# Optimization experiments

Measured on AMD Instinct MI355X. Metric: run time of the kernel, lower is better.

Reference implementation:

```python
import jax, jax.numpy as jnp
import numpy as np

B = 4          # per_gpu_batch_size
P = 16         # n_contexts
N = B * P      # fused passage dim = 64
L = 512        # seq_len
H = 768        # hidden_size
S = 16         # sentence spans per passage


def setup_inputs() -> dict:
    key = jax.random.key(0)
    k1, k2, k3 = jax.random.split(key, 3)
    hidden_states = jax.random.normal(k1, (N, L, H), jnp.float32)
    # nn.Linear weight [out, in]; original init std=1.0 saturates tanh, use 0.02 scale for sane numerics
    dense_w = jax.random.normal(k2, (H, H), jnp.float32) * 0.02
    dense_b = jnp.zeros((H,), jnp.float32)
    attention_mask = jnp.ones((N, L), jnp.int32)
    # strictly increasing boundaries -> S non-empty, ragged, contiguous spans per passage
    r = jnp.sort(jax.random.randint(k3, (N, S + 1), 0, L - S), axis=-1) + jnp.arange(S + 1, dtype=jnp.int32)
    spans = jnp.stack([r[:, :-1], r[:, 1:]], axis=-1).astype(jnp.int32)  # [N, S, 2]
    return dict(hidden_states=hidden_states, dense_w=dense_w, dense_b=dense_b,
                attention_mask=attention_mask, spans=spans)


def reference(hidden_states, dense_w, dense_b, attention_mask, spans):
    # sentence_spans branch: token_tensor = hidden_states (all tokens)
    # pooled_output = activation(dense(token_tensor)); cls_norm_type == 'none' -> no norm
    pooled = jnp.tanh(jnp.einsum('nlh,oh->nlo', hidden_states, dense_w) + dense_b)  # [N, L, H]
    pooled_output_passages = pooled[:, 0]  # [N, H]
    # ragged per-span mean pooling, vectorized as a masked segment reduce
    pos = jnp.arange(L, dtype=jnp.int32)                         # [L]
    start = spans[..., 0][..., None]                             # [N, S, 1]
    end = spans[..., 1][..., None]                               # [N, S, 1]
    m = ((pos >= start) & (pos < end)).astype(pooled.dtype)      # [N, S, L]
    sums = jnp.einsum('nsl,nlh->nsh', m, pooled)                 # [N, S, H]
    counts = (spans[..., 1] - spans[..., 0]).astype(pooled.dtype)[..., None]  # [N, S, 1]
    sentence_embeddings = (sums / counts).reshape(N * S, H)      # [N*S, H]
    # all S spans valid per passage -> mask of zeros (0 = valid in original code)
    sentence_mask = jnp.zeros((N, S), jnp.float32)
    return pooled_output_passages, sentence_embeddings, sentence_mask
```

## Files before the change

kernel.cpp:

```cpp
#include <hip/hip_runtime.h>
#include <hip/hip_bf16.h>

#define NPASS 64
#define LSEQ  512
#define HDIM  768
#define NSPAN 16
#define OFF_SENT (NPASS*HDIM)
#define OFF_MASK (OFF_SENT + NPASS*NSPAN*HDIM)

#define BN   96
#define NTN  6
#define BK   32
#define NK   (HDIM/BK)
#define NTILES (HDIM/BN)
#define NBLK (NPASS*NTILES)
#define THREADS 1024
#define NMT  2

typedef __bf16 bf16x8 __attribute__((ext_vector_type(8)));
typedef __bf16 bf16x4 __attribute__((ext_vector_type(4)));
typedef float  f32x4  __attribute__((ext_vector_type(4)));

__device__ inline float fast_tanh(float x) {
  const float ax = fabsf(x);
  const float t  = __expf(-2.0f * ax);
  const float r  = (1.0f - t) * __builtin_amdgcn_rcpf(1.0f + t);
  return copysignf(r, x);
}

__device__ inline bf16x8 cvt8(f32x4 lo, f32x4 hi) {
  union { bf16x4 h[2]; bf16x8 v; } u;
  u.h[0] = __builtin_convertvector(lo, bf16x4);
  u.h[1] = __builtin_convertvector(hi, bf16x4);
  return u.v;
}

__global__ __launch_bounds__(THREADS, 4) void fused_kernel(
    const float* __restrict__ A,
    const float* __restrict__ W,
    const float* __restrict__ bias,
    const int*   __restrict__ spans,
    float* __restrict__ out)
{
  __shared__ __align__(16) unsigned short Wl[BN * HDIM];
  __shared__ float sent_lds[NSPAN][BN];
  __shared__ float inv_s[NSPAN];
  __shared__ float bias_s[BN];
  __shared__ short sid_l[LSEQ];

  const int tid = threadIdx.x;
  const int b   = blockIdx.x;
  const int xcd = b & 7;
  const int t   = b >> 3;
  const int p   = ((t >> 3) << 3) | xcd;
  const int ntb = t & 7;
  const int tile_n = ntb * BN;


  {
    const float* Wp = W + (size_t)tile_n * HDIM;
    #pragma unroll
    for (int j = 0; j < (BN * (HDIM / 8)) / THREADS; ++j) {
      const int g  = j * THREADS + tid;
      const int wr = g / (HDIM / 8);
      const int kg = g % (HDIM / 8);
      const float* src = Wp + (size_t)wr * HDIM + kg * 8;
      const f32x4 lo = *(const f32x4*)src;
      const f32x4 hi = *(const f32x4*)(src + 4);
      const int kgs = kg ^ (wr & 7);
      *(bf16x8*)(Wl + (size_t)wr * HDIM + kgs * 8) = cvt8(lo, hi);
    }
  }

  if (tid < LSEQ) {
    int st[NSPAN], en[NSPAN];
    #pragma unroll
    for (int i = 0; i < NSPAN; ++i) {
      st[i] = spans[(p * NSPAN + i) * 2 + 0];
      en[i] = spans[(p * NSPAN + i) * 2 + 1];
    }
    short s = -1;
    #pragma unroll
    for (int i = 0; i < NSPAN; ++i)
      if (tid >= st[i] && tid < en[i]) s = (short)i;
    sid_l[tid] = s;
  }
  if (tid < NSPAN)
    inv_s[tid] = 1.0f / (float)(spans[(p * NSPAN + tid) * 2 + 1] -
                                spans[(p * NSPAN + tid) * 2 + 0]);
  if (tid >= 512 && tid < 512 + BN) bias_s[tid - 512] = bias[tile_n + tid - 512];
  for (int i = tid; i < NSPAN * BN; i += THREADS) (&sent_lds[0][0])[i] = 0.f;

  __syncthreads();

  const int wave = tid >> 6;
  const int lane = tid & 63;
  const int quad = lane >> 4;
  const int lr   = lane & 15;

  const float* Ab = A + ((size_t)p * LSEQ + wave * 32 + lr) * HDIM + quad * 8;

  f32x4 acc[NMT][NTN];
  #pragma unroll
  for (int mt = 0; mt < NMT; ++mt)
    #pragma unroll
    for (int nt = 0; nt < NTN; ++nt)
      acc[mt][nt] = (f32x4){0.f, 0.f, 0.f, 0.f};

  f32x4 alo[NMT], ahi[NMT];
  #pragma unroll
  for (int mt = 0; mt < NMT; ++mt) {
    const float* s0 = Ab + (size_t)mt * 16 * HDIM;
    alo[mt] = *(const f32x4*)s0;
    ahi[mt] = *(const f32x4*)(s0 + 4);
  }

  #pragma unroll
  for (int k = 0; k < NK; ++k) {
    bf16x8 wf[NTN];
    #pragma unroll
    for (int nt = 0; nt < NTN; ++nt) {
      const int wr = nt * 16 + lr;
      const int kg = (4 * k + quad) ^ (lr & 7);
      wf[nt] = *(const bf16x8*)(Wl + (size_t)wr * HDIM + kg * 8);
    }
    bf16x8 abf[NMT];
    #pragma unroll
    for (int mt = 0; mt < NMT; ++mt) abf[mt] = cvt8(alo[mt], ahi[mt]);
    if (k + 1 < NK) {
      #pragma unroll
      for (int mt = 0; mt < NMT; ++mt) {
        const float* s1 = Ab + (size_t)mt * 16 * HDIM + (k + 1) * BK;
        alo[mt] = *(const f32x4*)s1;
        ahi[mt] = *(const f32x4*)(s1 + 4);
      }
    }
    __builtin_amdgcn_s_setprio(1);
    #pragma unroll
    for (int mt = 0; mt < NMT; ++mt)
      #pragma unroll
      for (int nt = 0; nt < NTN; ++nt)
        acc[mt][nt] = __builtin_amdgcn_mfma_f32_16x16x32_bf16(
            abf[mt], wf[nt], acc[mt][nt], 0, 0, 0);
    __builtin_amdgcn_s_setprio(0);
  }

  #pragma unroll
  for (int nt = 0; nt < NTN; ++nt) {
    const int col = nt * 16 + lr;
    const float bv = bias_s[col];
    #pragma unroll
    for (int mt = 0; mt < NMT; ++mt) {
      const int rowbase = wave * 32 + mt * 16 + quad * 4;
      int prev = -1; float run = 0.f;
      #pragma unroll
      for (int r = 0; r < 4; ++r) {
        const int row = rowbase + r;
        const float v = fast_tanh(acc[mt][nt][r] + bv);
        if (row == 0) out[(size_t)p * HDIM + tile_n + col] = v;
        const int s = sid_l[row];
        if (s != prev) {
          if (prev >= 0) atomicAdd(&sent_lds[prev][col], run);
          prev = s; run = 0.f;
        }
        run += v;
      }
      if (prev >= 0) atomicAdd(&sent_lds[prev][col], run);
    }
  }
  __syncthreads();

  for (int i = tid; i < NSPAN * BN; i += THREADS) {
    const int s = i / BN, c = i % BN;
    out[OFF_SENT + ((size_t)p * NSPAN + s) * HDIM + tile_n + c] =
        sent_lds[s][c] * inv_s[s];
  }
  if (ntb == 0 && tid < NSPAN) out[OFF_MASK + p * NSPAN + tid] = 0.f;
}

extern "C" void kernel_launch(void* const* d_in, const int* in_sizes, int n_in,
                              void* d_out, int out_size, void* d_ws, size_t ws_size,
                              hipStream_t stream) {
  const float* hs  = (const float*)d_in[0];
  const float* w   = (const float*)d_in[1];
  const float* bsc = (const float*)d_in[2];
  const int* spans = (const int*)d_in[4];

  fused_kernel<<<dim3(NBLK), dim3(THREADS), 0, stream>>>(
      hs, w, bsc, spans, (float*)d_out);
}
```

Baseline: 228.8 us.

## Replace LDS atomic span accumulation with fp16 tile staging and serial span sums

```diff
diff --git a/kernel.cpp b/kernel.cpp
--- a/kernel.cpp
+++ b/kernel.cpp
@@ -1,5 +1,6 @@
 #include <hip/hip_runtime.h>
 #include <hip/hip_bf16.h>
+#include <hip/hip_fp16.h>
 
 #define NPASS 64
 #define LSEQ  512
@@ -16,6 +17,7 @@
 #define NBLK (NPASS*NTILES)
 #define THREADS 1024
 #define NMT  2
+#define PSTR 516
 
 typedef __bf16 bf16x8 __attribute__((ext_vector_type(8)));
 typedef __bf16 bf16x4 __attribute__((ext_vector_type(4)));
@@ -43,10 +45,9 @@
     float* __restrict__ out)
 {
   __shared__ __align__(16) unsigned short Wl[BN * HDIM];
-  __shared__ float sent_lds[NSPAN][BN];
+  __shared__ int   sp_st[NSPAN], sp_en[NSPAN];
   __shared__ float inv_s[NSPAN];
   __shared__ float bias_s[BN];
-  __shared__ short sid_l[LSEQ];
 
   const int tid = threadIdx.x;
   const int b   = blockIdx.x;
@@ -72,24 +73,13 @@
     }
   }
 
-  if (tid < LSEQ) {
-    int st[NSPAN], en[NSPAN];
-    #pragma unroll
-    for (int i = 0; i < NSPAN; ++i) {
-      st[i] = spans[(p * NSPAN + i) * 2 + 0];
-      en[i] = spans[(p * NSPAN + i) * 2 + 1];
-    }
-    short s = -1;
-    #pragma unroll
-    for (int i = 0; i < NSPAN; ++i)
-      if (tid >= st[i] && tid < en[i]) s = (short)i;
-    sid_l[tid] = s;
+  if (tid < NSPAN) {
+    const int st = spans[(p * NSPAN + tid) * 2 + 0];
+    const int en = spans[(p * NSPAN + tid) * 2 + 1];
+    sp_st[tid] = st; sp_en[tid] = en;
+    inv_s[tid] = 1.0f / (float)(en - st);
   }
-  if (tid < NSPAN)
-    inv_s[tid] = 1.0f / (float)(spans[(p * NSPAN + tid) * 2 + 1] -
-                                spans[(p * NSPAN + tid) * 2 + 0]);
   if (tid >= 512 && tid < 512 + BN) bias_s[tid - 512] = bias[tile_n + tid - 512];
-  for (int i = tid; i < NSPAN * BN; i += THREADS) (&sent_lds[0][0])[i] = 0.f;
 
   __syncthreads();
 
@@ -145,6 +135,9 @@
     __builtin_amdgcn_s_setprio(0);
   }
 
+  __syncthreads();
+  __half* P = reinterpret_cast<__half*>(Wl);
+
   #pragma unroll
   for (int nt = 0; nt < NTN; ++nt) {
     const int col = nt * 16 + lr;
@@ -152,29 +145,28 @@
     #pragma unroll
     for (int mt = 0; mt < NMT; ++mt) {
       const int rowbase = wave * 32 + mt * 16 + quad * 4;
-      int prev = -1; float run = 0.f;
-      #pragma unroll
-      for (int r = 0; r < 4; ++r) {
-        const int row = rowbase + r;
-        const float v = fast_tanh(acc[mt][nt][r] + bv);
-        if (row == 0) out[(size_t)p * HDIM + tile_n + col] = v;
-        const int s = sid_l[row];
-        if (s != prev) {
-          if (prev >= 0) atomicAdd(&sent_lds[prev][col], run);
-          prev = s; run = 0.f;
-        }
-        run += v;
-      }
-      if (prev >= 0) atomicAdd(&sent_lds[prev][col], run);
+      float v0 = fast_tanh(acc[mt][nt][0] + bv);
+      float v1 = fast_tanh(acc[mt][nt][1] + bv);
+      float v2 = fast_tanh(acc[mt][nt][2] + bv);
+      float v3 = fast_tanh(acc[mt][nt][3] + bv);
+      if (rowbase == 0) out[(size_t)p * HDIM + tile_n + col] = v0;
+      union { __half2 h2[2]; uint2 u; } pk;
+      pk.h2[0] = __floats2half2_rn(v0, v1);
+      pk.h2[1] = __floats2half2_rn(v2, v3);
+      *(uint2*)(P + (size_t)col * PSTR + rowbase) = pk.u;
     }
   }
   __syncthreads();
 
   for (int i = tid; i < NSPAN * BN; i += THREADS) {
     const int s = i / BN, c = i % BN;
-    out[OFF_SENT + ((size_t)p * NSPAN + s) * HDIM + tile_n + c] =
-        sent_lds[s][c] * inv_s[s];
+    const int st = sp_st[s], en = sp_en[s];
+    const __half* pc = P + (size_t)c * PSTR;
+    float sum = 0.f;
+    for (int r = st; r < en; ++r) sum += __half2float(pc[r]);
+    out[OFF_SENT + ((size_t)p * NSPAN + s) * HDIM + tile_n + c] = sum * inv_s[s];
   }
+
   if (ntb == 0 && tid < NSPAN) out[OFF_MASK + p * NSPAN + tid] = 0.f;
 }
 
```

After: 239.1 us. 1.05x slower.

## Double-buffer A register prefetch two K-steps ahead and overlap with W staging

Applied to the files above, without the earlier changes.

```diff
diff --git a/kernel.cpp b/kernel.cpp
--- a/kernel.cpp
+++ b/kernel.cpp
@@ -10,7 +10,7 @@
 
 #define BN   96
 #define NTN  6
-#define BK   32
+#define BK   64
 #define NK   (HDIM/BK)
 #define NTILES (HDIM/BN)
 #define NBLK (NPASS*NTILES)
@@ -56,6 +56,27 @@
   const int ntb = t & 7;
   const int tile_n = ntb * BN;
 
+  const int wave = tid >> 6;
+  const int lane = tid & 63;
+  const int quad = lane >> 4;
+  const int lr   = lane & 15;
+
+  const float* Ab = A + ((size_t)p * LSEQ + wave * 32 + lr) * HDIM + quad * 8;
+
+  f32x4 areg[2][NMT][4];
+  #define LOAD_A(q_, k_)                                                    \
+    _Pragma("unroll")                                                       \
+    for (int mt = 0; mt < NMT; ++mt) {                                      \
+      const float* s_ = Ab + (size_t)mt * 16 * HDIM + (k_) * BK;            \
+      _Pragma("unroll")                                                     \
+      for (int kk = 0; kk < 2; ++kk) {                                      \
+        areg[q_][mt][kk*2+0] = *(const f32x4*)(s_ + kk * 32);               \
+        areg[q_][mt][kk*2+1] = *(const f32x4*)(s_ + kk * 32 + 4);           \
+      }                                                                     \
+    }
+
+  LOAD_A(0, 0)
+  LOAD_A(1, 1)
 
   {
     const float* Wp = W + (size_t)tile_n * HDIM;
@@ -93,13 +114,6 @@
 
   __syncthreads();
 
-  const int wave = tid >> 6;
-  const int lane = tid & 63;
-  const int quad = lane >> 4;
-  const int lr   = lane & 15;
-
-  const float* Ab = A + ((size_t)p * LSEQ + wave * 32 + lr) * HDIM + quad * 8;
-
   f32x4 acc[NMT][NTN];
   #pragma unroll
   for (int mt = 0; mt < NMT; ++mt)
@@ -107,41 +121,40 @@
     for (int nt = 0; nt < NTN; ++nt)
       acc[mt][nt] = (f32x4){0.f, 0.f, 0.f, 0.f};
 
-  f32x4 alo[NMT], ahi[NMT];
-  #pragma unroll
-  for (int mt = 0; mt < NMT; ++mt) {
-    const float* s0 = Ab + (size_t)mt * 16 * HDIM;
-    alo[mt] = *(const f32x4*)s0;
-    ahi[mt] = *(const f32x4*)(s0 + 4);
-  }
-
   #pragma unroll
   for (int k = 0; k < NK; ++k) {
-    bf16x8 wf[NTN];
-    #pragma unroll
-    for (int nt = 0; nt < NTN; ++nt) {
-      const int wr = nt * 16 + lr;
-      const int kg = (4 * k + quad) ^ (lr & 7);
-      wf[nt] = *(const bf16x8*)(Wl + (size_t)wr * HDIM + kg * 8);
-    }
-    bf16x8 abf[NMT];
-    #pragma unroll
-    for (int mt = 0; mt < NMT; ++mt) abf[mt] = cvt8(alo[mt], ahi[mt]);
-    if (k + 1 < NK) {
-      #pragma unroll
-      for (int mt = 0; mt < NMT; ++mt) {
-        const float* s1 = Ab + (size_t)mt * 16 * HDIM + (k + 1) * BK;
-        alo[mt] = *(const f32x4*)s1;
-        ahi[mt] = *(const f32x4*)(s1 + 4);
+    const int q = k & 1;
+
+    bf16x8 wf[2][NTN];
+    #pragma unroll
+    for (int kk = 0; kk < 2; ++kk) {
+      const int ko = k * 2 + kk;
+      #pragma unroll
+      for (int nt = 0; nt < NTN; ++nt) {
+        const int wr = nt * 16 + lr;
+        const int kg = (4 * ko + quad) ^ (lr & 7);
+        wf[kk][nt] = *(const bf16x8*)(Wl + (size_t)wr * HDIM + kg * 8);
       }
     }
+
+    bf16x8 abf[2][NMT];
+    #pragma unroll
+    for (int kk = 0; kk < 2; ++kk)
+      #pragma unroll
+      for (int mt = 0; mt < NMT; ++mt)
+        abf[kk][mt] = cvt8(areg[q][mt][kk*2], areg[q][mt][kk*2+1]);
+
+    if (k + 2 < NK) { LOAD_A(q, k + 2) }
+
     __builtin_amdgcn_s_setprio(1);
     #pragma unroll
-    for (int mt = 0; mt < NMT; ++mt)
-      #pragma unroll
-      for (int nt = 0; nt < NTN; ++nt)
-        acc[mt][nt] = __builtin_amdgcn_mfma_f32_16x16x32_bf16(
-            abf[mt], wf[nt], acc[mt][nt], 0, 0, 0);
+    for (int kk = 0; kk < 2; ++kk)
+      #pragma unroll
+      for (int mt = 0; mt < NMT; ++mt)
+        #pragma unroll
+        for (int nt = 0; nt < NTN; ++nt)
+          acc[mt][nt] = __builtin_amdgcn_mfma_f32_16x16x32_bf16(
+              abf[kk][mt], wf[kk][nt], acc[mt][nt], 0, 0, 0);
     __builtin_amdgcn_s_setprio(0);
   }
 
```

Result: slower. 594.1 us (+159.7%).
